# Optimization experiments

Measured on AMD Instinct MI355X. Metric: run time of the kernel, lower is better.

Reference implementation:

```python
import jax, jax.numpy as jnp
import numpy as np

N_WAY, N_SHOT = 10, 15
N_QUERY, D = 8192, 1024
C_REG = 0.1
MAX_ITER = 15


def setup_inputs() -> dict:
    key = jax.random.key(0)
    k1, k2 = jax.random.split(key)
    n_sup = N_WAY * N_SHOT
    feat = jax.random.normal(k1, (n_sup + N_QUERY, D), dtype=jnp.float32) * 0.1
    label_support = jnp.arange(N_WAY, dtype=jnp.int32)
    label_query = jax.random.randint(k2, (N_QUERY,), 0, N_WAY, dtype=jnp.int32)
    scale = jnp.ones((1,), dtype=jnp.float32)
    return {"feat": feat, "label_support": label_support,
            "label_query": label_query, "scale": scale}


def _qp_solve(Q, p, h, A):
    """min 0.5 z'Qz + p'z  s.t.  z <= h,  A z = 0.
    Infeasible-start primal-dual interior-point method, MAX_ITER fixed iterations
    (mirrors qpth's QPFunction(maxIter=15) iterative batched-solve structure)."""
    n = Q.shape[0]
    m = A.shape[0]
    dtype = Q.dtype
    z = h - 1.0                      # slack s = h - z = 1 > 0
    s = jnp.ones((n,), dtype)
    lam = jnp.ones((n,), dtype)
    nu = jnp.zeros((m,), dtype)
    sigma = jnp.asarray(0.1, dtype)  # centering parameter

    def step(carry, _):
        z, s, lam, nu = carry
        mu = jnp.dot(s, lam) / n
        rd = Q @ z + p + lam + A.T @ nu      # dual residual
        rp = A @ z                           # primal (equality) residual, b = 0
        rc = s * lam - sigma * mu            # complementarity residual
        r1 = -rd + rc / s
        H = Q + jnp.diag(lam / s)
        L = jnp.linalg.cholesky(H)
        solveH = lambda r: jax.scipy.linalg.cho_solve((L, True), r)
        Hinv_AT = solveH(A.T)                # (n, m)
        Hinv_r1 = solveH(r1)                 # (n,)
        S = A @ Hinv_AT                      # (m, m) Schur complement
        dnu = jnp.linalg.solve(S, A @ Hinv_r1 + rp)
        dz = Hinv_r1 - Hinv_AT @ dnu
        ds = -dz
        dlam = (lam * dz - rc) / s

        def max_step(v, dv):                 # largest alpha keeping v + alpha*dv > 0
            ratios = jnp.where(dv < 0, -v / jnp.where(dv < 0, dv, -1.0), jnp.inf)
            return jnp.min(ratios)

        alpha = jnp.minimum(1.0, 0.99 * jnp.minimum(max_step(s, ds), max_step(lam, dlam)))
        return (z + alpha * dz, s + alpha * ds, lam + alpha * dlam, nu + alpha * dnu), None

    (z, s, lam, nu), _ = jax.lax.scan(step, (z, s, lam, nu), None, length=MAX_ITER)
    return z


def reference(feat, label_support, label_query, scale):
    n_way, n_shot = N_WAY, N_SHOT
    n_sup = n_way * n_shot
    support = feat[:n_sup]                       # (n_sup, d)
    query = feat[n_sup:]                         # (n_q, d)
    sup_labels = jnp.repeat(label_support, n_shot)   # label[0].repeat_interleave(n_shot)

    K = support @ support.T                      # Gram matrix (n_sup, n_sup)
    n = n_sup * n_way
    eye_w = jnp.eye(n_way, dtype=K.dtype)
    # batched_kronecker(K, I_way): index (i*n_way + a)
    Q = jnp.einsum('ij,ab->iajb', K, eye_w).reshape(n, n) + 10.0 * jnp.eye(n, dtype=K.dtype)
    y_onehot = jax.nn.one_hot(sup_labels, n_way, dtype=K.dtype).reshape(n)
    p = -y_onehot                                # e
    h = C_REG * y_onehot                         # box: z <= C_reg * Y (C = I)
    # A = kron(I_{n_sup}, ones(1, n_way))
    A = jnp.einsum('ij,a->ija', jnp.eye(n_sup, dtype=K.dtype),
                   jnp.ones((n_way,), K.dtype)).reshape(n_sup, n)

    qp_sol = _qp_solve(Q, p, h, A).reshape(n_sup, n_way)

    compat = support @ query.T                   # (n_sup, n_q)
    # logits[q, w] = sum_s compat[s, q] * qp_sol[s, w]
    logits = scale[0] * jnp.einsum('sq,sw->qw', compat, qp_sol)
    log_prb = jax.nn.log_softmax(logits, axis=1)     # (n_q, n_way)
    y_q = jax.nn.one_hot(label_query, n_way, dtype=log_prb.dtype)
    loss = -(y_q * log_prb).sum(axis=1).mean()
    return (log_prb, loss)
```

## Files before the change

kernel.cpp:

```cpp
#include <hip/hip_runtime.h>


#define NW    10
#define NSH   15
#define NSUP  150
#define NQ    8192
#define DIM   1024
#define NVAR  1500
#define NP    152
#define NTT   19
#define NACT  (NTT*NTT)
#define TPB   384
#define SIGMA 0.1f
#define PSTR  68

#define OFF_K     0
#define OFF_Z     22800
#define OFF_S     24300
#define OFF_LAM   25800
#define OFF_R1    27300
#define OFF_DZ    28800
#define OFF_DLAM  30300
#define OFF_G     31800
#define OFF_NU0   33300
#define OFF_NU1   33452
#define OFF_DNU   33604
#define OFF_DOTS  33756
#define OFF_MU    33786
#define OFF_SLOT  33788
#define OFF_LP    33792
#define OFF_WT    35840
#define OFF_SMAT  46080
#define OFF_X     69184
#define XSZ       (NP*NP)

__device__ __forceinline__ void bgj_core(float (&H)[8][8], const int t, const int tr, const int tc,
                                         float (*rowbuf)[PSTR], float (*colbuf)[NTT][PSTR],
                                         float (*wbuf)[PSTR]) {
  const int lane = t & 63;
  const int pr = lane >> 3, pc = lane & 7;
  const int r8 = t & 7;
  const int wj2 = t >> 3;
  const int jb = wj2 >> 1;
  const int jh4 = (wj2 & 1) << 2;
  const bool wact = (t < 8*NTT*2);
  const bool act = (t < NACT);
  for (int kb = 0; kb < NTT; ++kb) {
    const int cur = kb & 1, nxt = cur ^ 1;
    float p = rowbuf[kb][lane];
#pragma unroll
    for (int pp = 0; pp < 8; ++pp) {
      const float pv   = __shfl(p, pp*9, 64);
      const float d    = 1.0f / pv;
      const float rowv = __shfl(p, pp*8 + pc, 64);
      const float colv = __shfl(p, pr*8 + pp, 64);
      const float nr   = rowv * d;
      float v = fmaf(-colv, nr, p);
      if (pr == pp) v = nr;
      if (pc == pp) v = -colv * d;
      if (pr == pp && pc == pp) v = d;
      p = v;
    }
    float pv8[8];
#pragma unroll
    for (int q = 0; q < 8; ++q) pv8[q] = __shfl(p, r8*8 + q, 64);
    if (wact) {
      float w0, w1, w2, w3;
      if (jb == kb) {
        w0 = jh4 ? pv8[4] : pv8[0]; w1 = jh4 ? pv8[5] : pv8[1];
        w2 = jh4 ? pv8[6] : pv8[2]; w3 = jh4 ? pv8[7] : pv8[3];
      } else {
        w0 = w1 = w2 = w3 = 0.0f;
#pragma unroll
        for (int q = 0; q < 8; ++q) {
          const float4 x = *(const float4*)(&rowbuf[jb][q*8 + jh4]);
          w0 = fmaf(pv8[q], x.x, w0); w1 = fmaf(pv8[q], x.y, w1);
          w2 = fmaf(pv8[q], x.z, w2); w3 = fmaf(pv8[q], x.w, w3);
        }
      }
      *(float4*)(&wbuf[jb][r8*8 + jh4]) = make_float4(w0, w1, w2, w3);
    }
    __syncthreads();
    if (act) {
      if (tr == kb) {
        const float4* wsrc = (const float4*)(&wbuf[tc][0]);
#pragma unroll
        for (int r = 0; r < 8; ++r) {
          const float4 x = wsrc[2*r], y = wsrc[2*r+1];
          H[r][0]=x.x; H[r][1]=x.y; H[r][2]=x.z; H[r][3]=x.w;
          H[r][4]=y.x; H[r][5]=y.y; H[r][6]=y.z; H[r][7]=y.w;
        }
      } else {
        float C[8][8];
        const float4* cs = (const float4*)(&colbuf[cur][tr][0]);
#pragma unroll
        for (int r = 0; r < 8; ++r) {
          const float4 x = cs[2*r], y = cs[2*r+1];
          C[r][0]=x.x; C[r][1]=x.y; C[r][2]=x.z; C[r][3]=x.w;
          C[r][4]=y.x; C[r][5]=y.y; C[r][6]=y.z; C[r][7]=y.w;
        }
        if (tc == kb) {
#pragma unroll
          for (int r = 0; r < 8; ++r)
#pragma unroll
            for (int c = 0; c < 8; ++c) H[r][c] = 0.0f;
        }
        const float4* wsrc = (const float4*)(&wbuf[tc][0]);
#pragma unroll
        for (int q = 0; q < 8; ++q) {
          const float4 x = wsrc[2*q], y = wsrc[2*q+1];
          const float w0=x.x,w1=x.y,w2=x.z,w3=x.w,w4=y.x,w5=y.y,w6=y.z,w7=y.w;
#pragma unroll
          for (int r = 0; r < 8; ++r) {
            const float cq = C[r][q];
            H[r][0]=fmaf(-cq,w0,H[r][0]); H[r][1]=fmaf(-cq,w1,H[r][1]);
            H[r][2]=fmaf(-cq,w2,H[r][2]); H[r][3]=fmaf(-cq,w3,H[r][3]);
            H[r][4]=fmaf(-cq,w4,H[r][4]); H[r][5]=fmaf(-cq,w5,H[r][5]);
            H[r][6]=fmaf(-cq,w6,H[r][6]); H[r][7]=fmaf(-cq,w7,H[r][7]);
          }
        }
      }
      if (kb < NTT-1) {
        if (tr == kb+1) {
          float4* dst = (float4*)(&rowbuf[tc][0]);
#pragma unroll
          for (int r = 0; r < 8; ++r) {
            dst[2*r]   = make_float4(H[r][0],H[r][1],H[r][2],H[r][3]);
            dst[2*r+1] = make_float4(H[r][4],H[r][5],H[r][6],H[r][7]);
          }
        }
        if (tc == kb+1) {
          float4* dst = (float4*)(&colbuf[nxt][tr][0]);
#pragma unroll
          for (int r = 0; r < 8; ++r) {
            dst[2*r]   = make_float4(H[r][0],H[r][1],H[r][2],H[r][3]);
            dst[2*r+1] = make_float4(H[r][4],H[r][5],H[r][6],H[r][7]);
          }
        }
      }
    }
    __syncthreads();
  }
}

__global__ __launch_bounds__(256) void k_gram(const float* __restrict__ feat, float* __restrict__ ws) {
  const int bi = blockIdx.x / 10, bj = blockIdx.x % 10;
  const int t = threadIdx.x;
  const int r = t / 15, c = t % 15;
  const bool act = (t < 225);
  __shared__ float As[15][65], Bs[15][65];
  float acc = 0.0f;
  for (int ch = 0; ch < 16; ++ch) {
    for (int idx = t; idx < 960; idx += 256) {
      const int rr = idx >> 6, dd = idx & 63;
      As[rr][dd] = feat[(bi*15+rr)*DIM + ch*64 + dd];
      Bs[rr][dd] = feat[(bj*15+rr)*DIM + ch*64 + dd];
    }
    __syncthreads();
    if (act) {
      for (int dd = 0; dd < 64; ++dd) acc += As[r][dd] * Bs[c][dd];
    }
    __syncthreads();
  }
  if (act) ws[OFF_K + (bi*15+r)*NP + (bj*15+c)] = acc;
}

__global__ __launch_bounds__(TPB, 2) void kqpA(const int* __restrict__ labSup,
                                               float* __restrict__ ws, const int it) {
  const int b = blockIdx.x;
  const int t = threadIdx.x;
  const int tr = t / NTT, tc = t % NTT;
  const bool act = (t < NACT);
  __shared__ __align__(16) float rowbuf[NTT][PSTR], colbuf[2][NTT][PSTR], wbuf[NTT][PSTR];
  __shared__ float zloc[NP], sloc[NP], lloc[NP], dloc[NP], nuloc[NP], r1loc[NP];
  __shared__ float pacc[NP][NTT];
  unsigned* slots = (unsigned*)ws + OFF_SLOT;
  const int p = it & 1;
  float mu;
  if (it == 0) {
    if (t < NSUP) {
      const float y = (labSup[t/NSH] == b) ? 1.0f : 0.0f;
      const float zv = 0.1f*y - 1.0f;
      zloc[t] = zv; sloc[t] = 1.0f; lloc[t] = 1.0f; nuloc[t] = 0.0f;
      const int idx = t*NW + b;
      ws[OFF_Z+idx] = zv; ws[OFF_S+idx] = 1.0f; ws[OFF_LAM+idx] = 1.0f;
      if (b == 0) ws[OFF_NU1 + t] = 0.0f;
    } else if (t < NP) { zloc[t]=0.0f; sloc[t]=0.0f; lloc[t]=0.0f; nuloc[t]=0.0f; }
    mu = 1.0f;
    if (t == 0) slots[p] = 0x7F800000u;
    if (b == 0 && t == 0) ws[OFF_MU] = 1.0f;
  } else {
    const float am = __uint_as_float(slots[p^1]);
    const float alpha = fminf(1.0f, 0.99f * am);
    if (t == 0) slots[p] = 0x7F800000u;
    float D0 = 0.0f, D1 = 0.0f, D2 = 0.0f;
#pragma unroll
    for (int a = 0; a < NW; ++a) {
      D0 += ws[OFF_DOTS + a*3 + 0];
      D1 += ws[OFF_DOTS + a*3 + 1];
      D2 += ws[OFF_DOTS + a*3 + 2];
    }
    mu = (D0 + alpha*D1 - alpha*alpha*D2) / (float)NVAR;
    if (b == 0 && t == 0) ws[OFF_MU] = mu;
    const int nuR = OFF_NU0 + p*NP;
    const int nuW = OFF_NU0 + (p^1)*NP;
    if (t < NSUP) {
      const int idx = t*NW + b;
      const float dzv = ws[OFF_DZ + idx], dlv = ws[OFF_DLAM + idx];
      const float zn = ws[OFF_Z + idx]   + alpha*dzv;
      const float sn = ws[OFF_S + idx]   - alpha*dzv;
      const float ln = ws[OFF_LAM + idx] + alpha*dlv;
      ws[OFF_Z+idx]=zn; ws[OFF_S+idx]=sn; ws[OFF_LAM+idx]=ln;
      zloc[t]=zn; sloc[t]=sn; lloc[t]=ln;
      const float nv = ws[nuR + t] + alpha * ws[OFF_DNU + t];
      nuloc[t] = nv;
      if (b == 0) ws[nuW + t] = nv;
    } else if (t < NP) { zloc[t]=0.0f; sloc[t]=0.0f; lloc[t]=0.0f; nuloc[t]=0.0f; }
  }
  __syncthreads();
  if (t < NSUP) dloc[t] = lloc[t] / sloc[t];
  else if (t < NP) dloc[t] = 0.0f;
  __syncthreads();
  float H[8][8];
  if (act) {
#pragma unroll
    for (int r = 0; r < 8; ++r) {
      const int row = 8*tr + r;
      if (row < NSUP) {
        const float4* ks = (const float4*)(ws + OFF_K + row*NP + 8*tc);
        const float4 x = ks[0], y = ks[1];
        H[r][0]=x.x; H[r][1]=x.y; H[r][2]=x.z; H[r][3]=x.w;
        H[r][4]=y.x; H[r][5]=y.y; H[r][6]=y.z; H[r][7]=y.w;
        if (tc == NTT-1) { H[r][6] = 0.0f; H[r][7] = 0.0f; }
      } else {
#pragma unroll
        for (int c = 0; c < 8; ++c) H[r][c] = 0.0f;
      }
#pragma unroll
      for (int c = 0; c < 8; ++c) {
        const int col = 8*tc + c;
        if (col == row) H[r][c] += (row < NSUP) ? (10.0f + dloc[row]) : 1.0f;
      }
    }
#pragma unroll
    for (int r = 0; r < 8; ++r) {
      float pz = 0.0f;
#pragma unroll
      for (int c = 0; c < 8; ++c) pz = fmaf(H[r][c], zloc[8*tc + c], pz);
      pacc[8*tr + r][tc] = pz;
    }
    if (tr == 0) {
      float4* dst = (float4*)(&rowbuf[tc][0]);
#pragma unroll
      for (int r = 0; r < 8; ++r) {
        dst[2*r]   = make_float4(H[r][0],H[r][1],H[r][2],H[r][3]);
        dst[2*r+1] = make_float4(H[r][4],H[r][5],H[r][6],H[r][7]);
      }
    }
    if (tc == 0) {
      float4* dst = (float4*)(&colbuf[0][tr][0]);
#pragma unroll
      for (int r = 0; r < 8; ++r) {
        dst[2*r]   = make_float4(H[r][0],H[r][1],H[r][2],H[r][3]);
        dst[2*r+1] = make_float4(H[r][4],H[r][5],H[r][6],H[r][7]);
      }
    }
  }
  __syncthreads();
  if (t < NSUP) {
    float hz = 0.0f;
    for (int q = 0; q < NTT; ++q) hz += pacc[t][q];
    const float qz  = hz - dloc[t]*zloc[t];
    const float y   = (labSup[t/NSH] == b) ? 1.0f : 0.0f;
    const float rd  = qz - y + lloc[t] + nuloc[t];
    const float rc  = sloc[t]*lloc[t] - SIGMA*mu;
    const float r1v = -rd + rc/sloc[t];
    ws[OFF_R1 + t*NW + b] = r1v;
    r1loc[t] = r1v;
  } else if (t < NP) r1loc[t] = 0.0f;
  bgj_core(H, t, tr, tc, rowbuf, colbuf, wbuf);
  if (act) {
    float* Xb = ws + OFF_X + b*XSZ;
#pragma unroll
    for (int r = 0; r < 8; ++r) {
      float4* dst = (float4*)(Xb + (8*tr+r)*NP + 8*tc);
      dst[0] = make_float4(H[r][0],H[r][1],H[r][2],H[r][3]);
      dst[1] = make_float4(H[r][4],H[r][5],H[r][6],H[r][7]);
    }
#pragma unroll
    for (int r = 0; r < 8; ++r) {
      float pg = 0.0f;
#pragma unroll
      for (int c = 0; c < 8; ++c) pg = fmaf(H[r][c], r1loc[8*tc+c], pg);
      pacc[8*tr+r][tc] = pg;
    }
  }
  __syncthreads();
  if (t < NSUP) {
    float g = 0.0f;
    for (int q = 0; q < NTT; ++q) g += pacc[t][q];
    ws[OFF_G + t*NW + b] = g;
  }
}

__global__ __launch_bounds__(256) void k_sum(float* __restrict__ ws) {
  for (int idx = blockIdx.x*256 + threadIdx.x; idx < XSZ; idx += gridDim.x*256) {
    float v = 0.0f;
#pragma unroll
    for (int a = 0; a < NW; ++a) v += ws[OFF_X + a*XSZ + idx];
    ws[OFF_SMAT + idx] = v;
  }
}

__global__ __launch_bounds__(TPB, 2) void kqpB(float* __restrict__ ws, const int it) {
  const int b = blockIdx.x;
  const int t = threadIdx.x;
  const int tr = t / NTT, tc = t % NTT;
  const bool act = (t < NACT);
  __shared__ __align__(16) float rowbuf[NTT][PSTR], colbuf[2][NTT][PSTR], wbuf[NTT][PSTR];
  __shared__ float tloc[NP], r1l[NP], vloc[NP];
  __shared__ float pacc[NP][NTT];
  __shared__ float wred[TPB/64][3];
  const float mu = ws[OFF_MU];
  if (t < NP) {
    float v = 0.0f;
    if (t < NSUP) {
      float rp = 0.0f, gs = 0.0f;
#pragma unroll
      for (int a = 0; a < NW; ++a) {
        rp += ws[OFF_Z + t*NW + a];
        gs += ws[OFF_G + t*NW + a];
      }
      v = rp + gs;
      r1l[t] = ws[OFF_R1 + t*NW + b];
    } else r1l[t] = 0.0f;
    tloc[t] = v;
  }
  float Sg[8][8];
  if (act) {
#pragma unroll
    for (int r = 0; r < 8; ++r) {
      const float4* ss = (const float4*)(ws + OFF_SMAT + (8*tr+r)*NP + 8*tc);
      const float4 x = ss[0], y = ss[1];
      Sg[r][0]=x.x; Sg[r][1]=x.y; Sg[r][2]=x.z; Sg[r][3]=x.w;
      Sg[r][4]=y.x; Sg[r][5]=y.y; Sg[r][6]=y.z; Sg[r][7]=y.w;
    }
    if (tr == 0) {
      float4* dst = (float4*)(&rowbuf[tc][0]);
#pragma unroll
      for (int r = 0; r < 8; ++r) {
        dst[2*r]   = make_float4(Sg[r][0],Sg[r][1],Sg[r][2],Sg[r][3]);
        dst[2*r+1] = make_float4(Sg[r][4],Sg[r][5],Sg[r][6],Sg[r][7]);
      }
    }
    if (tc == 0) {
      float4* dst = (float4*)(&colbuf[0][tr][0]);
#pragma unroll
      for (int r = 0; r < 8; ++r) {
        dst[2*r]   = make_float4(Sg[r][0],Sg[r][1],Sg[r][2],Sg[r][3]);
        dst[2*r+1] = make_float4(Sg[r][4],Sg[r][5],Sg[r][6],Sg[r][7]);
      }
    }
  }
  __syncthreads();
  bgj_core(Sg, t, tr, tc, rowbuf, colbuf, wbuf);
  if (act) {
#pragma unroll
    for (int r = 0; r < 8; ++r) {
      float pd = 0.0f;
#pragma unroll
      for (int c = 0; c < 8; ++c) pd = fmaf(Sg[r][c], tloc[8*tc+c], pd);
      pacc[8*tr+r][tc] = pd;
    }
  }
  __syncthreads();
  if (t < NP) {
    float v = 0.0f;
    if (t < NSUP) {
      for (int q = 0; q < NTT; ++q) v += pacc[t][q];
      if (b == 0) ws[OFF_DNU + t] = v;
    }
    vloc[t] = (t < NSUP) ? (r1l[t] - v) : 0.0f;
  }
  __syncthreads();
  if (act) {
    const float* Xb = ws + OFF_X + b*XSZ;
    const int cb = 8*tc;
#pragma unroll
    for (int r = 0; r < 8; ++r) {
      const float4* src = (const float4*)(Xb + (8*tr+r)*NP + cb);
      const float4 v0 = src[0], v1 = src[1];
      pacc[8*tr+r][tc] =
          v0.x*vloc[cb+0] + v0.y*vloc[cb+1] + v0.z*vloc[cb+2] + v0.w*vloc[cb+3]
        + v1.x*vloc[cb+4] + v1.y*vloc[cb+5] + v1.z*vloc[cb+6] + v1.w*vloc[cb+7];
    }
  }
  __syncthreads();
  float d0 = 0.0f, d1 = 0.0f, d2 = 0.0f;
  if (t < NSUP) {
    float dzv = 0.0f;
    for (int q = 0; q < NTT; ++q) dzv += pacc[t][q];
    const int idx = t*NW + b;
    const float svv = ws[OFF_S + idx], lvv = ws[OFF_LAM + idx];
    const float rc  = svv*lvv - SIGMA*mu;
    const float dlv = (lvv*dzv - rc)/svv;
    ws[OFF_DZ + idx]   = dzv;
    ws[OFF_DLAM + idx] = dlv;
    unsigned* slot = (unsigned*)ws + OFF_SLOT + (it & 1);
    const float dsv = -dzv;
    if (dsv < 0.0f) atomicMin(slot, __float_as_uint(-svv/dsv));
    if (dlv < 0.0f) atomicMin(slot, __float_as_uint(-lvv/dlv));
    d0 = svv*lvv;
    d1 = svv*dlv - lvv*dzv;
    d2 = dzv*dlv;
  }
#pragma unroll
  for (int off = 32; off > 0; off >>= 1) {
    d0 += __shfl_xor(d0, off, 64);
    d1 += __shfl_xor(d1, off, 64);
    d2 += __shfl_xor(d2, off, 64);
  }
  if ((t & 63) == 0) { wred[t>>6][0]=d0; wred[t>>6][1]=d1; wred[t>>6][2]=d2; }
  __syncthreads();
  if (t == 0) {
    float s0=0.0f, s1=0.0f, s2=0.0f;
#pragma unroll
    for (int w = 0; w < TPB/64; ++w) { s0+=wred[w][0]; s1+=wred[w][1]; s2+=wred[w][2]; }
    ws[OFF_DOTS + b*3 + 0] = s0;
    ws[OFF_DOTS + b*3 + 1] = s1;
    ws[OFF_DOTS + b*3 + 2] = s2;
  }
}

__global__ __launch_bounds__(1024) void k_wt(const float* __restrict__ feat,
                                             const float* __restrict__ scale,
                                             float* __restrict__ ws) {
  const int w = blockIdx.x;
  const int dd = threadIdx.x;
  __shared__ float zloc[NSUP];
  const float am = __uint_as_float(((unsigned*)ws)[OFF_SLOT + 0]);
  const float alpha = fminf(1.0f, 0.99f * am);
  if (dd < NSUP) {
    const int idx = dd*NW + w;
    zloc[dd] = ws[OFF_Z + idx] + alpha * ws[OFF_DZ + idx];
  }
  __syncthreads();
  float acc = 0.0f;
  for (int ss = 0; ss < NSUP; ++ss)
    acc = fmaf(feat[(size_t)ss*DIM + dd], zloc[ss], acc);
  ws[OFF_WT + w*DIM + dd] = acc * scale[0];
}

__global__ __launch_bounds__(256) void k_logits(const float* __restrict__ feat,
                                                const int* __restrict__ labq,
                                                float* __restrict__ out,
                                                float* __restrict__ ws) {
  const int t = threadIdx.x;
  const int wv = t >> 6, l = t & 63;
  const int q = blockIdx.x*4 + wv;
  __shared__ float wtl[NW][DIM];
  __shared__ float lpart[4];
  for (int idx = t; idx < NW*DIM; idx += 256) wtl[idx >> 10][idx & 1023] = ws[OFF_WT + idx];
  __syncthreads();
  const float* qrow = feat + (size_t)(NSUP + q)*DIM;
  float acc[NW];
#pragma unroll
  for (int w = 0; w < NW; ++w) acc[w] = 0.0f;
#pragma unroll
  for (int c = 0; c < 4; ++c) {
    const float4 qv = *(const float4*)(qrow + c*256 + 4*l);
#pragma unroll
    for (int w = 0; w < NW; ++w) {
      const float4 wvv = *(const float4*)(&wtl[w][c*256 + 4*l]);
      acc[w] += qv.x*wvv.x + qv.y*wvv.y + qv.z*wvv.z + qv.w*wvv.w;
    }
  }
#pragma unroll
  for (int w = 0; w < NW; ++w) {
#pragma unroll
    for (int off = 32; off > 0; off >>= 1)
      acc[w] += __shfl_xor(acc[w], off, 64);
  }
  float m = acc[0];
#pragma unroll
  for (int w = 1; w < NW; ++w) m = fmaxf(m, acc[w]);
  float se = 0.0f;
#pragma unroll
  for (int w = 0; w < NW; ++w) se += expf(acc[w]-m);
  const float lse = m + logf(se);
  const int y = labq[q];
  if (l == 0) {
    float lpy = 0.0f;
#pragma unroll
    for (int w = 0; w < NW; ++w) {
      const float lp = acc[w] - lse;
      out[q*NW + w] = lp;
      if (w == y) lpy = lp;
    }
    lpart[wv] = -lpy;
  }
  __syncthreads();
  if (t == 0) ws[OFF_LP + blockIdx.x] = lpart[0]+lpart[1]+lpart[2]+lpart[3];
}

__global__ __launch_bounds__(1024) void k_loss(float* __restrict__ out, const float* __restrict__ ws) {
  const int t = threadIdx.x;
  __shared__ float red[1024];
  red[t] = ws[OFF_LP + t] + ws[OFF_LP + 1024 + t];
  __syncthreads();
  for (int off = 512; off > 0; off >>= 1) {
    if (t < off) red[t] += red[t + off];
    __syncthreads();
  }
  if (t == 0) out[NQ*NW] = red[0] / (float)NQ;
}

extern "C" void kernel_launch(void* const* d_in, const int* in_sizes, int n_in,
                              void* d_out, int out_size, void* d_ws, size_t ws_size,
                              hipStream_t stream) {
  const float* feat  = (const float*)d_in[0];
  const int*   labS  = (const int*)d_in[1];
  const int*   labQ  = (const int*)d_in[2];
  const float* scale = (const float*)d_in[3];
  float* ws  = (float*)d_ws;
  float* out = (float*)d_out;

  k_gram<<<100, 256, 0, stream>>>(feat, ws);
  for (int it = 0; it < 15; ++it) {
    kqpA<<<NW, TPB, 0, stream>>>(labS, ws, it);
    k_sum<<<32, 256, 0, stream>>>(ws);
    kqpB<<<NW, TPB, 0, stream>>>(ws, it);
  }
  k_wt<<<NW, 1024, 0, stream>>>(feat, scale, ws);
  k_logits<<<NQ/4, 256, 0, stream>>>(feat, labQ, out, ws);
  k_loss<<<1, 1024, 0, stream>>>(out, ws);
}
```

Measured before the change: 2.127 ms.

## Replace Schur block Gauss-Jordan inverse with block LU forward and back solve

In kqpB, the full block Gauss-Jordan inversion of the 152x152 Schur complement followed by a matrix-vector product is replaced by a block LU factorization that folds forward substitution into elimination (bglu_fwd), then a blocked back substitution. Only tiles on or right of the diagonal are updated, so roughly half the update FLOPs are skipped. The cost is a serial back-substitution loop of 19 steps with two block-wide barriers each, run by only a few threads.

```diff
diff --git a/kernel.cpp b/kernel.cpp
--- a/kernel.cpp
+++ b/kernel.cpp
@@ -117,6 +117,125 @@
             H[r][2]=fmaf(-cq,w2,H[r][2]); H[r][3]=fmaf(-cq,w3,H[r][3]);
             H[r][4]=fmaf(-cq,w4,H[r][4]); H[r][5]=fmaf(-cq,w5,H[r][5]);
             H[r][6]=fmaf(-cq,w6,H[r][6]); H[r][7]=fmaf(-cq,w7,H[r][7]);
+          }
+        }
+      }
+      if (kb < NTT-1) {
+        if (tr == kb+1) {
+          float4* dst = (float4*)(&rowbuf[tc][0]);
+#pragma unroll
+          for (int r = 0; r < 8; ++r) {
+            dst[2*r]   = make_float4(H[r][0],H[r][1],H[r][2],H[r][3]);
+            dst[2*r+1] = make_float4(H[r][4],H[r][5],H[r][6],H[r][7]);
+          }
+        }
+        if (tc == kb+1) {
+          float4* dst = (float4*)(&colbuf[nxt][tr][0]);
+#pragma unroll
+          for (int r = 0; r < 8; ++r) {
+            dst[2*r]   = make_float4(H[r][0],H[r][1],H[r][2],H[r][3]);
+            dst[2*r+1] = make_float4(H[r][4],H[r][5],H[r][6],H[r][7]);
+          }
+        }
+      }
+    }
+    __syncthreads();
+  }
+}
+
+__device__ __forceinline__ void bglu_fwd(float (&H)[8][8], const int t, const int tr, const int tc,
+                                         float (*rowbuf)[PSTR], float (*colbuf)[NTT][PSTR],
+                                         float (*wbuf)[PSTR], float* tvec, float* yvec) {
+  const int lane = t & 63;
+  const int pr = lane >> 3, pc = lane & 7;
+  const int r8 = t & 7;
+  const int wj2 = t >> 3;
+  const int jb = wj2 >> 1;
+  const int jh4 = (wj2 & 1) << 2;
+  const bool wact = (t < 8*NTT*2);
+  const bool act = (t < NACT);
+  for (int kb = 0; kb < NTT; ++kb) {
+    const int cur = kb & 1, nxt = cur ^ 1;
+    float p = rowbuf[kb][lane];
+#pragma unroll
+    for (int pp = 0; pp < 8; ++pp) {
+      const float pv   = __shfl(p, pp*9, 64);
+      const float d    = 1.0f / pv;
+      const float rowv = __shfl(p, pp*8 + pc, 64);
+      const float colv = __shfl(p, pr*8 + pp, 64);
+      const float nr   = rowv * d;
+      float v = fmaf(-colv, nr, p);
+      if (pr == pp) v = nr;
+      if (pc == pp) v = -colv * d;
+      if (pr == pp && pc == pp) v = d;
+      p = v;
+    }
+    float pv8[8];
+#pragma unroll
+    for (int q = 0; q < 8; ++q) pv8[q] = __shfl(p, r8*8 + q, 64);
+    if (wact && jb >= kb) {
+      float w0, w1, w2, w3;
+      if (jb == kb) {
+        w0 = jh4 ? pv8[4] : pv8[0]; w1 = jh4 ? pv8[5] : pv8[1];
+        w2 = jh4 ? pv8[6] : pv8[2]; w3 = jh4 ? pv8[7] : pv8[3];
+      } else {
+        w0 = w1 = w2 = w3 = 0.0f;
+#pragma unroll
+        for (int q = 0; q < 8; ++q) {
+          const float4 x = *(const float4*)(&rowbuf[jb][q*8 + jh4]);
+          w0 = fmaf(pv8[q], x.x, w0); w1 = fmaf(pv8[q], x.y, w1);
+          w2 = fmaf(pv8[q], x.z, w2); w3 = fmaf(pv8[q], x.w, w3);
+        }
+      }
+      *(float4*)(&wbuf[jb][r8*8 + jh4]) = make_float4(w0, w1, w2, w3);
+    }
+    if (t < 8) {
+      float yv = 0.0f;
+#pragma unroll
+      for (int q = 0; q < 8; ++q) yv = fmaf(pv8[q], tvec[kb*8+q], yv);
+      yvec[kb*8 + r8] = yv;
+    }
+    __syncthreads();
+    if (act) {
+      if (tr == kb) {
+        const float4* wsrc = (const float4*)(&wbuf[tc][0]);
+#pragma unroll
+        for (int r = 0; r < 8; ++r) {
+          const float4 x = wsrc[2*r], y = wsrc[2*r+1];
+          H[r][0]=x.x; H[r][1]=x.y; H[r][2]=x.z; H[r][3]=x.w;
+          H[r][4]=y.x; H[r][5]=y.y; H[r][6]=y.z; H[r][7]=y.w;
+        }
+      } else if (tr > kb) {
+        if (tc == kb) {
+#pragma unroll
+          for (int r = 0; r < 8; ++r) {
+            float s = 0.0f;
+#pragma unroll
+            for (int c = 0; c < 8; ++c) s = fmaf(H[r][c], yvec[kb*8+c], s);
+            tvec[tr*8+r] -= s;
+          }
+        } else if (tc > kb) {
+          float C[8][8];
+          const float4* cs = (const float4*)(&colbuf[cur][tr][0]);
+#pragma unroll
+          for (int r = 0; r < 8; ++r) {
+            const float4 x = cs[2*r], y = cs[2*r+1];
+            C[r][0]=x.x; C[r][1]=x.y; C[r][2]=x.z; C[r][3]=x.w;
+            C[r][4]=y.x; C[r][5]=y.y; C[r][6]=y.z; C[r][7]=y.w;
+          }
+          const float4* wsrc = (const float4*)(&wbuf[tc][0]);
+#pragma unroll
+          for (int q = 0; q < 8; ++q) {
+            const float4 x = wsrc[2*q], y = wsrc[2*q+1];
+            const float w0=x.x,w1=x.y,w2=x.z,w3=x.w,w4=y.x,w5=y.y,w6=y.z,w7=y.w;
+#pragma unroll
+            for (int r = 0; r < 8; ++r) {
+              const float cq = C[r][q];
+              H[r][0]=fmaf(-cq,w0,H[r][0]); H[r][1]=fmaf(-cq,w1,H[r][1]);
+              H[r][2]=fmaf(-cq,w2,H[r][2]); H[r][3]=fmaf(-cq,w3,H[r][3]);
+              H[r][4]=fmaf(-cq,w4,H[r][4]); H[r][5]=fmaf(-cq,w5,H[r][5]);
+              H[r][6]=fmaf(-cq,w6,H[r][6]); H[r][7]=fmaf(-cq,w7,H[r][7]);
+            }
           }
         }
       }
@@ -318,7 +437,7 @@
   const int tr = t / NTT, tc = t % NTT;
   const bool act = (t < NACT);
   __shared__ __align__(16) float rowbuf[NTT][PSTR], colbuf[2][NTT][PSTR], wbuf[NTT][PSTR];
-  __shared__ float tloc[NP], r1l[NP], vloc[NP];
+  __shared__ float tvec[NP], yvec[NP], xvec[NP], r1l[NP], vloc[NP];
   __shared__ float pacc[NP][NTT];
   __shared__ float wred[TPB/64][3];
   const float mu = ws[OFF_MU];
@@ -334,7 +453,7 @@
       v = rp + gs;
       r1l[t] = ws[OFF_R1 + t*NW + b];
     } else r1l[t] = 0.0f;
-    tloc[t] = v;
+    tvec[t] = v;
   }
   float Sg[8][8];
   if (act) {
@@ -363,25 +482,30 @@
     }
   }
   __syncthreads();
-  bgj_core(Sg, t, tr, tc, rowbuf, colbuf, wbuf);
-  if (act) {
-#pragma unroll
-    for (int r = 0; r < 8; ++r) {
-      float pd = 0.0f;
-#pragma unroll
-      for (int c = 0; c < 8; ++c) pd = fmaf(Sg[r][c], tloc[8*tc+c], pd);
-      pacc[8*tr+r][tc] = pd;
-    }
-  }
-  __syncthreads();
-  if (t < NP) {
-    float v = 0.0f;
-    if (t < NSUP) {
-      for (int q = 0; q < NTT; ++q) v += pacc[t][q];
-      if (b == 0) ws[OFF_DNU + t] = v;
-    }
-    vloc[t] = (t < NSUP) ? (r1l[t] - v) : 0.0f;
-  }
+  bglu_fwd(Sg, t, tr, tc, rowbuf, colbuf, wbuf, tvec, yvec);
+  for (int kb = NTT-1; kb >= 0; --kb) {
+    if (act && tr == kb && tc > kb) {
+      float xr[8];
+#pragma unroll
+      for (int c = 0; c < 8; ++c) xr[c] = xvec[tc*8 + c];
+#pragma unroll
+      for (int r = 0; r < 8; ++r) {
+        float s = 0.0f;
+#pragma unroll
+        for (int c = 0; c < 8; ++c) s = fmaf(Sg[r][c], xr[c], s);
+        pacc[r][tc] = s;
+      }
+    }
+    __syncthreads();
+    if (t < 8) {
+      float s = yvec[kb*8 + t];
+      for (int j = kb+1; j < NTT; ++j) s -= pacc[t][j];
+      xvec[kb*8 + t] = s;
+    }
+    __syncthreads();
+  }
+  if (b == 0 && t < NSUP) ws[OFF_DNU + t] = xvec[t];
+  if (t < NP) vloc[t] = (t < NSUP) ? (r1l[t] - xvec[t]) : 0.0f;
   __syncthreads();
   if (act) {
     const float* Xb = ws + OFF_X + b*XSZ;
```

New measurement: 2.226 ms. +4.6%, slower.

## Pack two QP classes per kqpA block and compute matvecs via row dot products

Applied to the files above, without the earlier changes.

kqpA now launches 5 blocks of 768 threads, each half handling one class, instead of 10 blocks of 384. The H·z and H^-1·r1 matvecs drop the shared partial-sum array and its reduction barriers. Instead, each row thread dots directly against K or the stored inverse read back from global memory. This removes shared arrays and a few syncthreads, at the cost of halving the block count and adding global reads, and it relies on written X being visible after a block barrier.

```diff
diff --git a/kernel.cpp b/kernel.cpp
--- a/kernel.cpp
+++ b/kernel.cpp
@@ -10,6 +10,8 @@
 #define NP    152
 #define NTT   19
 #define NACT  (NTT*NTT)
+#define HALF  384
+#define TPBA  768
 #define TPB   384
 #define SIGMA 0.1f
 #define PSTR  68
@@ -165,34 +167,38 @@
   if (act) ws[OFF_K + (bi*15+r)*NP + (bj*15+c)] = acc;
 }
 
-__global__ __launch_bounds__(TPB, 2) void kqpA(const int* __restrict__ labSup,
-                                               float* __restrict__ ws, const int it) {
-  const int b = blockIdx.x;
+__global__ __launch_bounds__(TPBA, 1) void kqpA(const int* __restrict__ labSup,
+                                                float* __restrict__ ws, const int it) {
   const int t = threadIdx.x;
-  const int tr = t / NTT, tc = t % NTT;
-  const bool act = (t < NACT);
-  __shared__ __align__(16) float rowbuf[NTT][PSTR], colbuf[2][NTT][PSTR], wbuf[NTT][PSTR];
-  __shared__ float zloc[NP], sloc[NP], lloc[NP], dloc[NP], nuloc[NP], r1loc[NP];
-  __shared__ float pacc[NP][NTT];
+  const int half = (t >= HALF) ? 1 : 0;
+  const int th = t - half*HALF;
+  const int b = blockIdx.x*2 + half;
+  const int tr = th / NTT, tc = th % NTT;
+  const bool act = (th < NACT);
+  __shared__ __align__(16) float rowbuf[2][NTT][PSTR];
+  __shared__ __align__(16) float colbuf[2][2][NTT][PSTR];
+  __shared__ __align__(16) float wbuf[2][NTT][PSTR];
+  __shared__ float zloc[2][NP], dloc[2][NP], r1loc[2][NP];
   unsigned* slots = (unsigned*)ws + OFF_SLOT;
   const int p = it & 1;
   float mu;
+  float zv = 0.0f, sv = 1.0f, lv = 1.0f, nv = 0.0f;
   if (it == 0) {
-    if (t < NSUP) {
-      const float y = (labSup[t/NSH] == b) ? 1.0f : 0.0f;
-      const float zv = 0.1f*y - 1.0f;
-      zloc[t] = zv; sloc[t] = 1.0f; lloc[t] = 1.0f; nuloc[t] = 0.0f;
-      const int idx = t*NW + b;
+    mu = 1.0f;
+    if (th == 0) slots[p] = 0x7F800000u;
+    if (b == 0 && th == 0) ws[OFF_MU] = 1.0f;
+    if (th < NSUP) {
+      const float y = (labSup[th/NSH] == b) ? 1.0f : 0.0f;
+      zv = 0.1f*y - 1.0f; sv = 1.0f; lv = 1.0f; nv = 0.0f;
+      const int idx = th*NW + b;
       ws[OFF_Z+idx] = zv; ws[OFF_S+idx] = 1.0f; ws[OFF_LAM+idx] = 1.0f;
-      if (b == 0) ws[OFF_NU1 + t] = 0.0f;
-    } else if (t < NP) { zloc[t]=0.0f; sloc[t]=0.0f; lloc[t]=0.0f; nuloc[t]=0.0f; }
-    mu = 1.0f;
-    if (t == 0) slots[p] = 0x7F800000u;
-    if (b == 0 && t == 0) ws[OFF_MU] = 1.0f;
+      if (b == 0) ws[OFF_NU1 + th] = 0.0f;
+      zloc[half][th] = zv; dloc[half][th] = 1.0f;
+    } else if (th < NP) { zloc[half][th] = 0.0f; dloc[half][th] = 0.0f; }
   } else {
     const float am = __uint_as_float(slots[p^1]);
     const float alpha = fminf(1.0f, 0.99f * am);
-    if (t == 0) slots[p] = 0x7F800000u;
+    if (th == 0) slots[p] = 0x7F800000u;
     float D0 = 0.0f, D1 = 0.0f, D2 = 0.0f;
 #pragma unroll
     for (int a = 0; a < NW; ++a) {
@@ -201,25 +207,22 @@
       D2 += ws[OFF_DOTS + a*3 + 2];
     }
     mu = (D0 + alpha*D1 - alpha*alpha*D2) / (float)NVAR;
-    if (b == 0 && t == 0) ws[OFF_MU] = mu;
+    if (b == 0 && th == 0) ws[OFF_MU] = mu;
     const int nuR = OFF_NU0 + p*NP;
     const int nuW = OFF_NU0 + (p^1)*NP;
-    if (t < NSUP) {
-      const int idx = t*NW + b;
+    if (th < NSUP) {
+      const int idx = th*NW + b;
       const float dzv = ws[OFF_DZ + idx], dlv = ws[OFF_DLAM + idx];
-      const float zn = ws[OFF_Z + idx]   + alpha*dzv;
-      const float sn = ws[OFF_S + idx]   - alpha*dzv;
-      const float ln = ws[OFF_LAM + idx] + alpha*dlv;
-      ws[OFF_Z+idx]=zn; ws[OFF_S+idx]=sn; ws[OFF_LAM+idx]=ln;
-      zloc[t]=zn; sloc[t]=sn; lloc[t]=ln;
-      const float nv = ws[nuR + t] + alpha * ws[OFF_DNU + t];
-      nuloc[t] = nv;
-      if (b == 0) ws[nuW + t] = nv;
-    } else if (t < NP) { zloc[t]=0.0f; sloc[t]=0.0f; lloc[t]=0.0f; nuloc[t]=0.0f; }
-  }
-  __syncthreads();
-  if (t < NSUP) dloc[t] = lloc[t] / sloc[t];
-  else if (t < NP) dloc[t] = 0.0f;
+      zv = ws[OFF_Z + idx]   + alpha*dzv;
+      sv = ws[OFF_S + idx]   - alpha*dzv;
+      lv = ws[OFF_LAM + idx] + alpha*dlv;
+      ws[OFF_Z+idx]=zv; ws[OFF_S+idx]=sv; ws[OFF_LAM+idx]=lv;
+      nv = ws[nuR + th] + alpha * ws[OFF_DNU + th];
+      if (b == 0) ws[nuW + th] = nv;
+      zloc[half][th] = zv; dloc[half][th] = lv/sv;
+    } else if (th < NP) { zloc[half][th] = 0.0f; dloc[half][th] = 0.0f; }
+  }
+  if (th >= NSUP && th < NP) r1loc[half][th] = 0.0f;
   __syncthreads();
   float H[8][8];
   if (act) {
@@ -239,18 +242,11 @@
 #pragma unroll
       for (int c = 0; c < 8; ++c) {
         const int col = 8*tc + c;
-        if (col == row) H[r][c] += (row < NSUP) ? (10.0f + dloc[row]) : 1.0f;
-      }
-    }
-#pragma unroll
-    for (int r = 0; r < 8; ++r) {
-      float pz = 0.0f;
-#pragma unroll
-      for (int c = 0; c < 8; ++c) pz = fmaf(H[r][c], zloc[8*tc + c], pz);
-      pacc[8*tr + r][tc] = pz;
+        if (col == row) H[r][c] += (row < NSUP) ? (10.0f + dloc[half][row]) : 1.0f;
+      }
     }
     if (tr == 0) {
-      float4* dst = (float4*)(&rowbuf[tc][0]);
+      float4* dst = (float4*)(&rowbuf[half][tc][0]);
 #pragma unroll
       for (int r = 0; r < 8; ++r) {
         dst[2*r]   = make_float4(H[r][0],H[r][1],H[r][2],H[r][3]);
@@ -258,7 +254,7 @@
       }
     }
     if (tc == 0) {
-      float4* dst = (float4*)(&colbuf[0][tr][0]);
+      float4* dst = (float4*)(&colbuf[half][0][tr][0]);
 #pragma unroll
       for (int r = 0; r < 8; ++r) {
         dst[2*r]   = make_float4(H[r][0],H[r][1],H[r][2],H[r][3]);
@@ -266,19 +262,26 @@
       }
     }
   }
-  __syncthreads();
-  if (t < NSUP) {
+  if (th < NSUP) {
+    const float* Krow = ws + OFF_K + th*NP;
     float hz = 0.0f;
-    for (int q = 0; q < NTT; ++q) hz += pacc[t][q];
-    const float qz  = hz - dloc[t]*zloc[t];
-    const float y   = (labSup[t/NSH] == b) ? 1.0f : 0.0f;
-    const float rd  = qz - y + lloc[t] + nuloc[t];
-    const float rc  = sloc[t]*lloc[t] - SIGMA*mu;
-    const float r1v = -rd + rc/sloc[t];
-    ws[OFF_R1 + t*NW + b] = r1v;
-    r1loc[t] = r1v;
-  } else if (t < NP) r1loc[t] = 0.0f;
-  bgj_core(H, t, tr, tc, rowbuf, colbuf, wbuf);
+    for (int j = 0; j < NP; j += 4) {
+      const float4 k4 = *(const float4*)(Krow + j);
+      hz = fmaf(k4.x, zloc[half][j+0], hz);
+      hz = fmaf(k4.y, zloc[half][j+1], hz);
+      hz = fmaf(k4.z, zloc[half][j+2], hz);
+      hz = fmaf(k4.w, zloc[half][j+3], hz);
+    }
+    const float qz  = hz + 10.0f*zv;
+    const float y   = (labSup[th/NSH] == b) ? 1.0f : 0.0f;
+    const float rd  = qz - y + lv + nv;
+    const float rc  = sv*lv - SIGMA*mu;
+    const float r1v = -rd + rc/sv;
+    ws[OFF_R1 + th*NW + b] = r1v;
+    r1loc[half][th] = r1v;
+  }
+  __syncthreads();
+  bgj_core(H, th, tr, tc, rowbuf[half], colbuf[half], wbuf[half]);
   if (act) {
     float* Xb = ws + OFF_X + b*XSZ;
 #pragma unroll
@@ -287,19 +290,19 @@
       dst[0] = make_float4(H[r][0],H[r][1],H[r][2],H[r][3]);
       dst[1] = make_float4(H[r][4],H[r][5],H[r][6],H[r][7]);
     }
-#pragma unroll
-    for (int r = 0; r < 8; ++r) {
-      float pg = 0.0f;
-#pragma unroll
-      for (int c = 0; c < 8; ++c) pg = fmaf(H[r][c], r1loc[8*tc+c], pg);
-      pacc[8*tr+r][tc] = pg;
-    }
-  }
-  __syncthreads();
-  if (t < NSUP) {
+  }
+  __syncthreads();
+  if (th < NSUP) {
+    const float* Xrow = ws + OFF_X + b*XSZ + th*NP;
     float g = 0.0f;
-    for (int q = 0; q < NTT; ++q) g += pacc[t][q];
-    ws[OFF_G + t*NW + b] = g;
+    for (int j = 0; j < NP; j += 4) {
+      const float4 x4 = *(const float4*)(Xrow + j);
+      g = fmaf(x4.x, r1loc[half][j+0], g);
+      g = fmaf(x4.y, r1loc[half][j+1], g);
+      g = fmaf(x4.z, r1loc[half][j+2], g);
+      g = fmaf(x4.w, r1loc[half][j+3], g);
+    }
+    ws[OFF_G + th*NW + b] = g;
   }
 }
 
@@ -527,7 +530,7 @@
 
   k_gram<<<100, 256, 0, stream>>>(feat, ws);
   for (int it = 0; it < 15; ++it) {
-    kqpA<<<NW, TPB, 0, stream>>>(labS, ws, it);
+    kqpA<<<NW/2, TPBA, 0, stream>>>(labS, ws, it);
     k_sum<<<32, 256, 0, stream>>>(ws);
     kqpB<<<NW, TPB, 0, stream>>>(ws, it);
   }
```

New measurement: 2.728 ms. +28.2%, slower.
